# Kernel optimization log

Hardware: AMD Instinct MI355X
Metric: run time of the kernel (lower is better)

## Reference

```python
import jax, jax.numpy as jnp
import numpy as np

ITERN = 5  # hard-coded SqrtmLayer(cov_mat, 5)


def setup_inputs() -> dict:
    key = jax.random.key(0)
    k1, k2, k3 = jax.random.split(key, 3)
    B, C, H, W = 16, 64, 256, 256
    R = 8  # reduction
    x = jax.random.normal(k1, (B, C, H, W), dtype=jnp.float32)
    w1 = jax.random.normal(k2, (C // R, C), dtype=jnp.float32) * 0.1
    b1 = jnp.zeros((C // R,), dtype=jnp.float32)
    w2 = jax.random.normal(k3, (C, C // R), dtype=jnp.float32) * 0.1
    b2 = jnp.zeros((C,), dtype=jnp.float32)
    return {"x": x, "w1": w1, "b1": b1, "w2": w2, "b2": b2}


def _covpool(x):
    # x: [B, C, h, w].  y = x @ I_hat @ x^T with I_hat = (1/M)I - (1/M^2)J,
    # which equals centered covariance: (x_c @ x_c^T) / M.
    B, C, h, w = x.shape
    M = h * w
    xf = x.reshape(B, C, M)
    xc = xf - jnp.mean(xf, axis=-1, keepdims=True)
    return jnp.einsum('bcm,bdm->bcd', xc, xc) / M  # [B, C, C]


def _sqrtm_ns(cov, iterN):
    # Newton-Schulz iteration for matrix square root (per-batch [C,C]).
    B, C, _ = cov.shape
    I = jnp.eye(C, dtype=cov.dtype)
    I3 = 3.0 * I
    normA = jnp.einsum('bii->b', cov)  # trace
    A = cov / normA[:, None, None]
    ZY = 0.5 * (I3 - A)
    Y = jnp.matmul(A, ZY)
    Z = ZY
    for _ in range(1, iterN - 1):
        ZY = 0.5 * (I3 - jnp.matmul(Z, Y))
        Y = jnp.matmul(Y, ZY)
        Z = jnp.matmul(ZY, Z)
    ZY = 0.5 * jnp.matmul(Y, I3 - jnp.matmul(Z, Y))
    return ZY * jnp.sqrt(normA)[:, None, None]


def reference(x, w1, b1, w2, b2):
    # h,w < 1000 so the crop branch is identity (x_sub = x)
    cov = _covpool(x)                       # [B, C, C]
    cov_sqrt = _sqrtm_ns(cov, ITERN)        # [B, C, C]
    v = jnp.mean(cov_sqrt, axis=1)          # [B, C] (mean over rows, dim=1)
    hid = jax.nn.relu(jnp.einsum('bc,hc->bh', v, w1) + b1)
    att = jax.nn.sigmoid(jnp.einsum('bh,ch->bc', hid, w2) + b2)
    return att[:, :, None, None] * x
```

## Files before the change

kernel.cpp:

```cpp
#include <hip/hip_runtime.h>
#include <hip/hip_bf16.h>
#include <math.h>

#define BATCH 16
#define CH    64
#define MM    65536
#define PSTRIDE 4160
#define SF    68

typedef __attribute__((ext_vector_type(8))) short s16x8;
typedef __attribute__((ext_vector_type(4))) float f32x4;

__device__ __forceinline__ unsigned short f2bf(float f) {
    __hip_bfloat16 h = __float2bfloat16(f);
    return __builtin_bit_cast(unsigned short, h);
}
__device__ __forceinline__ float bf2f(unsigned short u) {
    return __builtin_bit_cast(float, (unsigned)u << 16);
}

__global__ __launch_bounds__(256, 3) void gram_mfma(const float* __restrict__ x,
                                                    float* __restrict__ part,
                                                    int nchunk, int chunk_m) {
    int blk = blockIdx.x;
    int b = blk / nchunk, chunk = blk - b * nchunk;
    int t = threadIdx.x, w = t >> 6, l = t & 63;
    int lr = l & 15, lg = l >> 4;
    int mwave = chunk_m >> 2;
    int nck = mwave >> 5;

    const float* xw = x + (size_t)b * CH * MM + (size_t)chunk * chunk_m +
                      (size_t)w * mwave + lg * 8;
    const float* rp0 = xw + (size_t)(lr)      * MM;
    const float* rp1 = xw + (size_t)(16 + lr) * MM;
    const float* rp2 = xw + (size_t)(32 + lr) * MM;
    const float* rp3 = xw + (size_t)(48 + lr) * MM;

    f32x4 acc[10];
    f32x4 accs[4];
    const f32x4 zero = {0.f, 0.f, 0.f, 0.f};
#pragma unroll
    for (int i = 0; i < 10; ++i) acc[i] = zero;
#pragma unroll
    for (int i = 0; i < 4; ++i) accs[i] = zero;

    s16x8 ones;
    {
        unsigned short* op1 = (unsigned short*)&ones;
#pragma unroll
        for (int i = 0; i < 8; ++i) op1[i] = 0x3F80;
    }

    float4 A0, A1, A2, A3, A4, A5, A6, A7;
    float4 B0, B1, B2, B3, B4, B5, B6, B7;

#define LOAD8(P, o) do {                                                      \
        P##0 = *(const float4*)(rp0 + (o));  P##1 = *(const float4*)(rp0 + (o) + 4); \
        P##2 = *(const float4*)(rp1 + (o));  P##3 = *(const float4*)(rp1 + (o) + 4); \
        P##4 = *(const float4*)(rp2 + (o));  P##5 = *(const float4*)(rp2 + (o) + 4); \
        P##6 = *(const float4*)(rp3 + (o));  P##7 = *(const float4*)(rp3 + (o) + 4); \
    } while (0)

#define CVT_ROW(va, vb, fr) do {                                              \
        unsigned short* fp = (unsigned short*)&(fr);                          \
        fp[0] = f2bf((va).x); fp[1] = f2bf((va).y);                           \
        fp[2] = f2bf((va).z); fp[3] = f2bf((va).w);                           \
        fp[4] = f2bf((vb).x); fp[5] = f2bf((vb).y);                           \
        fp[6] = f2bf((vb).z); fp[7] = f2bf((vb).w);                           \
    } while (0)

#define COMPUTE(P) do {                                                       \
        s16x8 fr0, fr1, fr2, fr3;                                             \
        CVT_ROW(P##0, P##1, fr0);                                             \
        CVT_ROW(P##2, P##3, fr1);                                             \
        CVT_ROW(P##4, P##5, fr2);                                             \
        CVT_ROW(P##6, P##7, fr3);                                             \
        acc[0] = __builtin_amdgcn_mfma_f32_16x16x32_bf16(fr0, fr0, acc[0], 0, 0, 0); \
        acc[1] = __builtin_amdgcn_mfma_f32_16x16x32_bf16(fr0, fr1, acc[1], 0, 0, 0); \
        acc[2] = __builtin_amdgcn_mfma_f32_16x16x32_bf16(fr0, fr2, acc[2], 0, 0, 0); \
        acc[3] = __builtin_amdgcn_mfma_f32_16x16x32_bf16(fr0, fr3, acc[3], 0, 0, 0); \
        acc[4] = __builtin_amdgcn_mfma_f32_16x16x32_bf16(fr1, fr1, acc[4], 0, 0, 0); \
        acc[5] = __builtin_amdgcn_mfma_f32_16x16x32_bf16(fr1, fr2, acc[5], 0, 0, 0); \
        acc[6] = __builtin_amdgcn_mfma_f32_16x16x32_bf16(fr1, fr3, acc[6], 0, 0, 0); \
        acc[7] = __builtin_amdgcn_mfma_f32_16x16x32_bf16(fr2, fr2, acc[7], 0, 0, 0); \
        acc[8] = __builtin_amdgcn_mfma_f32_16x16x32_bf16(fr2, fr3, acc[8], 0, 0, 0); \
        acc[9] = __builtin_amdgcn_mfma_f32_16x16x32_bf16(fr3, fr3, acc[9], 0, 0, 0); \
        accs[0] = __builtin_amdgcn_mfma_f32_16x16x32_bf16(ones, fr0, accs[0], 0, 0, 0); \
        accs[1] = __builtin_amdgcn_mfma_f32_16x16x32_bf16(ones, fr1, accs[1], 0, 0, 0); \
        accs[2] = __builtin_amdgcn_mfma_f32_16x16x32_bf16(ones, fr2, accs[2], 0, 0, 0); \
        accs[3] = __builtin_amdgcn_mfma_f32_16x16x32_bf16(ones, fr3, accs[3], 0, 0, 0); \
    } while (0)

    LOAD8(A, 0);
    for (int c = 0; c < nck; c += 2) {
        LOAD8(B, (c + 1) * 32);
        COMPUTE(A);
        if (c + 2 < nck) LOAD8(A, (c + 2) * 32);
        COMPUTE(B);
    }

#define UIDX(i, j) ((i) * 4 + (j) - ((i) * ((i) + 1)) / 2)

    __shared__ float xs[64 * 65];
    __shared__ float csum[64];
    for (int ww = 0; ww < 4; ++ww) {
        if (w == ww) {
#pragma unroll
            for (int i = 0; i < 4; ++i)
#pragma unroll
                for (int j = 0; j < 4; ++j)
                    if (i <= j) {
#pragma unroll
                        for (int jj = 0; jj < 4; ++jj) {
                            int r = i * 16 + lg * 4 + jj, cc = j * 16 + lr;
                            float v = acc[UIDX(i, j)][jj];
                            if (ww == 0) xs[r * 65 + cc] = v;
                            else         xs[r * 65 + cc] += v;
                        }
                    }
            if (l < 16) {
                if (ww == 0) {
                    csum[l]      = accs[0][0]; csum[16 + l] = accs[1][0];
                    csum[32 + l] = accs[2][0]; csum[48 + l] = accs[3][0];
                } else {
                    csum[l]      += accs[0][0]; csum[16 + l] += accs[1][0];
                    csum[32 + l] += accs[2][0]; csum[48 + l] += accs[3][0];
                }
            }
        }
        __syncthreads();
    }

    float* op = part + (size_t)blk * PSTRIDE;
#pragma unroll
    for (int rix = 0; rix < 16; ++rix) {
        int e = t + rix * 256;
        int r = e >> 6, cc = e & 63;
        float v = ((r >> 4) > (cc >> 4)) ? xs[cc * 65 + r] : xs[r * 65 + cc];
        __builtin_nontemporal_store(v, op + e);
    }
    if (t < 64) __builtin_nontemporal_store(csum[t], op + 4096 + t);
}

__global__ __launch_bounds__(256) void reduce_parts(const float* __restrict__ part,
                                                    float* __restrict__ red,
                                                    int nchunk) {
    int b = blockIdx.y;
    int i = blockIdx.x * 256 + threadIdx.x;
    if (i >= PSTRIDE / 4) return;
    const f32x4* p = reinterpret_cast<const f32x4*>(part + (size_t)b * nchunk * PSTRIDE) + i;
    f32x4 s = {0.f, 0.f, 0.f, 0.f};
    for (int ch = 0; ch < nchunk; ++ch) {
        f32x4 v = __builtin_nontemporal_load(p + (size_t)ch * (PSTRIDE / 4));
        s += v;
    }
    reinterpret_cast<f32x4*>(red + (size_t)b * PSTRIDE)[i] = s;
}

__device__ __forceinline__ void cvt_store(const float* __restrict__ M, int row,
                                          int col, unsigned short* Hp,
                                          unsigned short* Lp) {
    float4 v = *reinterpret_cast<const float4*>(M + row * SF + col);
    ushort4 h, lo;
    h.x = f2bf(v.x); lo.x = f2bf(v.x - bf2f(h.x));
    h.y = f2bf(v.y); lo.y = f2bf(v.y - bf2f(h.y));
    h.z = f2bf(v.z); lo.z = f2bf(v.z - bf2f(h.z));
    h.w = f2bf(v.w); lo.w = f2bf(v.w - bf2f(h.w));
    int byte = (row * 128 + col * 2) ^ ((row & 7) << 4);
    *reinterpret_cast<ushort4*>(reinterpret_cast<char*>(Hp) + byte) = h;
    *reinterpret_cast<ushort4*>(reinterpret_cast<char*>(Lp) + byte) = lo;
}

template <int EPI>
__device__ __forceinline__ void mm64(const float* __restrict__ A,
                                     const float* __restrict__ B,
                                     float* __restrict__ C,
                                     unsigned short* AHp, unsigned short* ALp,
                                     unsigned short* BHp, unsigned short* BLp,
                                     int t) {
    int w = t >> 6, l = t & 63, lg = l >> 4, lr = l & 15;
    __syncthreads();
#pragma unroll
    for (int r = 0; r < 4; ++r) {
        int e4 = t + r * 256;
        int row = e4 >> 4;
        int col = (e4 & 15) << 2;
        cvt_store(A, row, col, AHp, ALp);
        cvt_store(B, row, col, BHp, BLp);
    }
    __syncthreads();
    f32x4 acc[4];
    const f32x4 zero = {0.f, 0.f, 0.f, 0.f};
#pragma unroll
    for (int i = 0; i < 4; ++i) acc[i] = zero;
    int arow = w * 16 + lr;
#pragma unroll
    for (int kk = 0; kk < 2; ++kk) {
        int kbyte = kk * 64 + lg * 16;
        int abyte = (arow * 128 + kbyte) ^ ((arow & 7) << 4);
        s16x8 ah = *reinterpret_cast<const s16x8*>(reinterpret_cast<const char*>(AHp) + abyte);
        s16x8 al = *reinterpret_cast<const s16x8*>(reinterpret_cast<const char*>(ALp) + abyte);
#pragma unroll
        for (int ct = 0; ct < 4; ++ct) {
            int brow = ct * 16 + lr;
            int bbyte = (brow * 128 + kbyte) ^ ((brow & 7) << 4);
            s16x8 bh = *reinterpret_cast<const s16x8*>(reinterpret_cast<const char*>(BHp) + bbyte);
            s16x8 bl = *reinterpret_cast<const s16x8*>(reinterpret_cast<const char*>(BLp) + bbyte);
            acc[ct] = __builtin_amdgcn_mfma_f32_16x16x32_bf16(ah, bh, acc[ct], 0, 0, 0);
            acc[ct] = __builtin_amdgcn_mfma_f32_16x16x32_bf16(ah, bl, acc[ct], 0, 0, 0);
            acc[ct] = __builtin_amdgcn_mfma_f32_16x16x32_bf16(al, bh, acc[ct], 0, 0, 0);
        }
    }
#pragma unroll
    for (int ct = 0; ct < 4; ++ct)
#pragma unroll
        for (int j = 0; j < 4; ++j) {
            int r = w * 16 + lg * 4 + j, c = ct * 16 + lr;
            float v = acc[ct][j];
            if (EPI == 1) v = (r == c ? 1.5f : 0.f) - 0.5f * v;
            C[r * SF + c] = v;
        }
    __syncthreads();
}

__device__ __forceinline__ void mv64(float* __restrict__ dst,
                                     const float* __restrict__ M,
                                     const float* __restrict__ src,
                                     float* __restrict__ mvp, int t) {
    int i = t & 63, q = t >> 6;
    float p = 0.f;
#pragma unroll
    for (int jj = 0; jj < 16; ++jj) {
        int j = q * 16 + jj;
        float s = src ? src[j] : 1.f;
        p = fmaf(M[j * SF + i], s, p);
    }
    mvp[q * 64 + i] = p;
    __syncthreads();
    if (t < 64) dst[t] = (mvp[t] + mvp[64 + t]) + (mvp[128 + t] + mvp[192 + t]);
    __syncthreads();
}

__global__ __launch_bounds__(256) void ns_att(const float* __restrict__ red,
                                              const float* __restrict__ w1,
                                              const float* __restrict__ b1,
                                              const float* __restrict__ w2,
                                              const float* __restrict__ b2,
                                              float* __restrict__ att) {
    __shared__ float BUF[5][64 * SF];
    __shared__ unsigned short AH[64 * 64], AL[64 * 64], BH[64 * 64], BL[64 * 64];
    __shared__ float sv[64], u4s[64], vecA[64], vecB[64];
    __shared__ float mvp[256];
    __shared__ float hid8[8];
    __shared__ float scal[2];

    int b = blockIdx.x, t = threadIdx.x;
    const float* pb = red + (size_t)b * PSTRIDE;

    if (t < 64) sv[t] = pb[4096 + t];
    __syncthreads();

    const float invM = 1.0f / (float)MM;
    const float invM2 = invM * invM;
#pragma unroll
    for (int r = 0; r < 4; ++r) {
        int e4 = t + r * 256;
        int row = e4 >> 4;
        int col = (e4 & 15) << 2;
        float4 g = *(reinterpret_cast<const float4*>(pb) + e4);
        float sr = sv[row] * invM2;
        BUF[0][row * SF + col]     = g.x * invM - sr * sv[col];
        BUF[0][row * SF + col + 1] = g.y * invM - sr * sv[col + 1];
        BUF[0][row * SF + col + 2] = g.z * invM - sr * sv[col + 2];
        BUF[0][row * SF + col + 3] = g.w * invM - sr * sv[col + 3];
    }
    __syncthreads();

    if (t < 64) {
        float d = BUF[0][t * SF + t];
#pragma unroll
        for (int m = 1; m < 64; m <<= 1) d += __shfl_xor(d, m);
        if (t == 0) { scal[0] = 1.0f / d; scal[1] = sqrtf(d); }
    }
    __syncthreads();
    float itr = scal[0];

#pragma unroll
    for (int rr = 0; rr < 16; ++rr) {
        int e = t + rr * 256;
        int r = e >> 6, c = e & 63;
        float a = BUF[0][r * SF + c] * itr;
        BUF[0][r * SF + c] = a;
        BUF[1][r * SF + c] = (r == c ? 1.5f : 0.f) - 0.5f * a;
    }

    mm64<0>(BUF[0], BUF[1], BUF[2], AH, AL, BH, BL, t);
    mm64<1>(BUF[1], BUF[2], BUF[3], AH, AL, BH, BL, t);
    mm64<0>(BUF[2], BUF[3], BUF[4], AH, AL, BH, BL, t);
    mm64<0>(BUF[3], BUF[1], BUF[0], AH, AL, BH, BL, t);
    mm64<1>(BUF[0], BUF[4], BUF[1], AH, AL, BH, BL, t);
    mm64<0>(BUF[4], BUF[1], BUF[2], AH, AL, BH, BL, t);
    mm64<0>(BUF[1], BUF[0], BUF[3], AH, AL, BH, BL, t);
    mm64<1>(BUF[3], BUF[2], BUF[0], AH, AL, BH, BL, t);

    mv64(vecA, BUF[2], nullptr, mvp, t);
    mv64(u4s,  BUF[0], vecA,    mvp, t);
    mv64(vecA, BUF[0], u4s,     mvp, t);
    mv64(vecB, BUF[3], vecA,    mvp, t);
    mv64(vecA, BUF[2], vecB,    mvp, t);
    mv64(vecB, BUF[0], vecA,    mvp, t);

    if (t < 64) sv[t] = (1.5f * u4s[t] - 0.5f * vecB[t]) * scal[1] * (1.0f / 64.0f);
    __syncthreads();
    if (t < 8) {
        float h = b1[t];
        for (int c = 0; c < 64; ++c) h += sv[c] * w1[t * 64 + c];
        hid8[t] = h > 0.f ? h : 0.f;
    }
    __syncthreads();
    if (t < 64) {
        float p = b2[t];
        for (int h = 0; h < 8; ++h) p += hid8[h] * w2[t * 8 + h];
        att[b * 64 + t] = 1.0f / (1.0f + expf(-p));
    }
}

__global__ __launch_bounds__(256) void scale_out(const float* __restrict__ x,
                                                 const float* __restrict__ att,
                                                 float* __restrict__ out) {
    const size_t total4 = (size_t)BATCH * CH * MM / 4;
    const size_t stride = (size_t)gridDim.x * blockDim.x;
    const f32x4* x4 = reinterpret_cast<const f32x4*>(x);
    f32x4* o4 = reinterpret_cast<f32x4*>(out);
    size_t base = (size_t)(gridDim.x - 1 - blockIdx.x) * blockDim.x + threadIdx.x;
    int niter = (int)(total4 / stride);
    size_t i = base + (size_t)(niter - 1) * stride;
    for (int k = 0; k < niter; ++k) {
        int bc = (int)(i >> 14);
        float a = att[bc];
        f32x4 v = x4[i];
        v *= a;
        __builtin_nontemporal_store(v, o4 + i);
        i -= stride;
    }
}

extern "C" void kernel_launch(void* const* d_in, const int* in_sizes, int n_in,
                              void* d_out, int out_size, void* d_ws, size_t ws_size,
                              hipStream_t stream) {
    const float* x  = (const float*)d_in[0];
    const float* w1 = (const float*)d_in[1];
    const float* b1 = (const float*)d_in[2];
    const float* w2 = (const float*)d_in[3];
    const float* b2 = (const float*)d_in[4];
    float* out = (float*)d_out;
    float* ws  = (float*)d_ws;

    int nchunk = 64;
    for (;;) {
        size_t need = ((size_t)BATCH * nchunk * PSTRIDE + (size_t)BATCH * PSTRIDE +
                       (size_t)BATCH * CH) * sizeof(float);
        if (need <= ws_size || nchunk == 1) break;
        nchunk >>= 1;
    }
    int chunk_m = MM / nchunk;

    float* part = ws;
    float* red  = ws + (size_t)BATCH * nchunk * PSTRIDE;
    float* att  = red + (size_t)BATCH * PSTRIDE;

    gram_mfma<<<BATCH * nchunk, 256, 0, stream>>>(x, part, nchunk, chunk_m);
    reduce_parts<<<dim3((PSTRIDE / 4 + 255) / 256, BATCH), 256, 0, stream>>>(part, red, nchunk);
    ns_att<<<BATCH, 256, 0, stream>>>(red, w1, b1, w2, b2, att);
    scale_out<<<4096, 256, 0, stream>>>(x, att, out);
}
```

Measured before the change: 173.0 us.

## Stash bf16 copy of x during Gram pass and scale from it

The Gram kernel now writes the bf16-converted input tiles it already builds for the MFMAs into a workspace buffer. The final scaling kernel then reads that half-width copy instead of the fp32 input. The goal is to cut the read traffic of the last elementwise pass; input loads also become nontemporal. In exchange the Gram pass writes an extra half-size copy of x, so total memory traffic is roughly unchanged. The output also loses precision because it is computed from bf16-rounded x, and the path only runs when the workspace can hold the copy, otherwise it falls back to the old kernels.

```diff
diff --git a/kernel.cpp b/kernel.cpp
--- a/kernel.cpp
+++ b/kernel.cpp
@@ -19,8 +19,10 @@
     return __builtin_bit_cast(float, (unsigned)u << 16);
 }
 
+template <int WC>
 __global__ __launch_bounds__(256, 3) void gram_mfma(const float* __restrict__ x,
                                                     float* __restrict__ part,
+                                                    unsigned short* __restrict__ xb16,
                                                     int nchunk, int chunk_m) {
     int blk = blockIdx.x;
     int b = blk / nchunk, chunk = blk - b * nchunk;
@@ -35,6 +37,10 @@
     const float* rp1 = xw + (size_t)(16 + lr) * MM;
     const float* rp2 = xw + (size_t)(32 + lr) * MM;
     const float* rp3 = xw + (size_t)(48 + lr) * MM;
+    unsigned short* cp0 = xb16 + (size_t)(rp0 - x);
+    unsigned short* cp1 = xb16 + (size_t)(rp1 - x);
+    unsigned short* cp2 = xb16 + (size_t)(rp2 - x);
+    unsigned short* cp3 = xb16 + (size_t)(rp3 - x);
 
     f32x4 acc[10];
     f32x4 accs[4];
@@ -51,30 +57,40 @@
         for (int i = 0; i < 8; ++i) op1[i] = 0x3F80;
     }
 
-    float4 A0, A1, A2, A3, A4, A5, A6, A7;
-    float4 B0, B1, B2, B3, B4, B5, B6, B7;
+    f32x4 A0, A1, A2, A3, A4, A5, A6, A7;
+    f32x4 B0, B1, B2, B3, B4, B5, B6, B7;
 
 #define LOAD8(P, o) do {                                                      \
-        P##0 = *(const float4*)(rp0 + (o));  P##1 = *(const float4*)(rp0 + (o) + 4); \
-        P##2 = *(const float4*)(rp1 + (o));  P##3 = *(const float4*)(rp1 + (o) + 4); \
-        P##4 = *(const float4*)(rp2 + (o));  P##5 = *(const float4*)(rp2 + (o) + 4); \
-        P##6 = *(const float4*)(rp3 + (o));  P##7 = *(const float4*)(rp3 + (o) + 4); \
+        P##0 = __builtin_nontemporal_load(reinterpret_cast<const f32x4*>(rp0 + (o)));     \
+        P##1 = __builtin_nontemporal_load(reinterpret_cast<const f32x4*>(rp0 + (o) + 4)); \
+        P##2 = __builtin_nontemporal_load(reinterpret_cast<const f32x4*>(rp1 + (o)));     \
+        P##3 = __builtin_nontemporal_load(reinterpret_cast<const f32x4*>(rp1 + (o) + 4)); \
+        P##4 = __builtin_nontemporal_load(reinterpret_cast<const f32x4*>(rp2 + (o)));     \
+        P##5 = __builtin_nontemporal_load(reinterpret_cast<const f32x4*>(rp2 + (o) + 4)); \
+        P##6 = __builtin_nontemporal_load(reinterpret_cast<const f32x4*>(rp3 + (o)));     \
+        P##7 = __builtin_nontemporal_load(reinterpret_cast<const f32x4*>(rp3 + (o) + 4)); \
     } while (0)
 
 #define CVT_ROW(va, vb, fr) do {                                              \
         unsigned short* fp = (unsigned short*)&(fr);                          \
-        fp[0] = f2bf((va).x); fp[1] = f2bf((va).y);                           \
-        fp[2] = f2bf((va).z); fp[3] = f2bf((va).w);                           \
-        fp[4] = f2bf((vb).x); fp[5] = f2bf((vb).y);                           \
-        fp[6] = f2bf((vb).z); fp[7] = f2bf((vb).w);                           \
+        fp[0] = f2bf((va)[0]); fp[1] = f2bf((va)[1]);                         \
+        fp[2] = f2bf((va)[2]); fp[3] = f2bf((va)[3]);                         \
+        fp[4] = f2bf((vb)[0]); fp[5] = f2bf((vb)[1]);                         \
+        fp[6] = f2bf((vb)[2]); fp[7] = f2bf((vb)[3]);                         \
     } while (0)
 
-#define COMPUTE(P) do {                                                       \
+#define COMPUTE(P, o) do {                                                    \
         s16x8 fr0, fr1, fr2, fr3;                                             \
         CVT_ROW(P##0, P##1, fr0);                                             \
         CVT_ROW(P##2, P##3, fr1);                                             \
         CVT_ROW(P##4, P##5, fr2);                                             \
         CVT_ROW(P##6, P##7, fr3);                                             \
+        if (WC) {                                                             \
+            *reinterpret_cast<s16x8*>(cp0 + (o)) = fr0;                       \
+            *reinterpret_cast<s16x8*>(cp1 + (o)) = fr1;                       \
+            *reinterpret_cast<s16x8*>(cp2 + (o)) = fr2;                       \
+            *reinterpret_cast<s16x8*>(cp3 + (o)) = fr3;                       \
+        }                                                                     \
         acc[0] = __builtin_amdgcn_mfma_f32_16x16x32_bf16(fr0, fr0, acc[0], 0, 0, 0); \
         acc[1] = __builtin_amdgcn_mfma_f32_16x16x32_bf16(fr0, fr1, acc[1], 0, 0, 0); \
         acc[2] = __builtin_amdgcn_mfma_f32_16x16x32_bf16(fr0, fr2, acc[2], 0, 0, 0); \
@@ -94,9 +110,9 @@
     LOAD8(A, 0);
     for (int c = 0; c < nck; c += 2) {
         LOAD8(B, (c + 1) * 32);
-        COMPUTE(A);
+        COMPUTE(A, c * 32);
         if (c + 2 < nck) LOAD8(A, (c + 2) * 32);
-        COMPUTE(B);
+        COMPUTE(B, (c + 1) * 32);
     }
 
 #define UIDX(i, j) ((i) * 4 + (j) - ((i) * ((i) + 1)) / 2)
@@ -325,6 +341,26 @@
     }
 }
 
+__global__ __launch_bounds__(256) void scale_copy(const unsigned short* __restrict__ xc,
+                                                  const float* __restrict__ att,
+                                                  float* __restrict__ out) {
+    const size_t total4 = (size_t)BATCH * CH * MM / 4;
+    const size_t stride = (size_t)gridDim.x * blockDim.x;
+    f32x4* o4 = reinterpret_cast<f32x4*>(out);
+    size_t j = (size_t)blockIdx.x * blockDim.x + threadIdx.x;
+    for (; j < total4; j += stride) {
+        int bc = (int)(j >> 14);
+        float a = att[bc];
+        ushort4 u = *reinterpret_cast<const ushort4*>(xc + 4 * j);
+        f32x4 v;
+        v[0] = bf2f(u.x) * a;
+        v[1] = bf2f(u.y) * a;
+        v[2] = bf2f(u.z) * a;
+        v[3] = bf2f(u.w) * a;
+        __builtin_nontemporal_store(v, o4 + j);
+    }
+}
+
 __global__ __launch_bounds__(256) void scale_out(const float* __restrict__ x,
                                                  const float* __restrict__ att,
                                                  float* __restrict__ out) {
@@ -354,23 +390,32 @@
     const float* w2 = (const float*)d_in[3];
     const float* b2 = (const float*)d_in[4];
     float* out = (float*)d_out;
-    float* ws  = (float*)d_ws;
-
-    int nchunk = 64;
-    for (;;) {
-        size_t need = ((size_t)BATCH * nchunk * PSTRIDE + (size_t)BATCH * PSTRIDE +
-                       (size_t)BATCH * CH) * sizeof(float);
-        if (need <= ws_size || nchunk == 1) break;
-        nchunk >>= 1;
-    }
-    int chunk_m = MM / nchunk;
-
-    float* part = ws;
-    float* red  = ws + (size_t)BATCH * nchunk * PSTRIDE;
-    float* att  = red + (size_t)BATCH * PSTRIDE;
-
-    gram_mfma<<<BATCH * nchunk, 256, 0, stream>>>(x, part, nchunk, chunk_m);
+
+    const int nchunk = 64;
+    const int chunk_m = MM / nchunk;
+    const size_t copy_bytes = (size_t)BATCH * CH * MM * 2;
+    const size_t part_bytes = (size_t)BATCH * nchunk * PSTRIDE * 4;
+    const size_t red_bytes  = (size_t)BATCH * PSTRIDE * 4;
+    const size_t att_bytes  = (size_t)BATCH * CH * 4;
+
+    bool wc = ws_size >= copy_bytes + part_bytes + red_bytes + att_bytes;
+
+    char* wsb = (char*)d_ws;
+    unsigned short* xb16 = (unsigned short*)wsb;
+    float* part = (float*)(wsb + (wc ? copy_bytes : 0));
+    float* red  = (float*)((char*)part + part_bytes);
+    float* att  = (float*)((char*)red + red_bytes);
+
+    if (wc) {
+        gram_mfma<1><<<BATCH * nchunk, 256, 0, stream>>>(x, part, xb16, nchunk, chunk_m);
+    } else {
+        gram_mfma<0><<<BATCH * nchunk, 256, 0, stream>>>(x, part, xb16, nchunk, chunk_m);
+    }
     reduce_parts<<<dim3((PSTRIDE / 4 + 255) / 256, BATCH), 256, 0, stream>>>(part, red, nchunk);
     ns_att<<<BATCH, 256, 0, stream>>>(red, w1, b1, w2, b2, att);
-    scale_out<<<4096, 256, 0, stream>>>(x, att, out);
-}
+    if (wc) {
+        scale_copy<<<4096, 256, 0, stream>>>(xb16, att, out);
+    } else {
+        scale_out<<<4096, 256, 0, stream>>>(x, att, out);
+    }
+}
```

After: 197.3 us. 14.0% more time.
